# Optimization experiments

Hardware: AMD Instinct MI355X
Metric: run time of the kernel (lower is better)

Reference implementation:

```python
import jax, jax.numpy as jnp
import numpy as np

N = 50000        # num nodes
E = 800000       # num edges (avg degree 16)
IN = 64          # in_channels
H = 128          # hidden_channels
C1 = 64          # Num_TCN (fine clusters)
C2 = 16          # Num_TCN2 (coarse clusters)
DROP = 0.5       # drop_rate
THRESH = 1.0 / (C1 - 1)  # default edge_pruning_threshold
LN_EPS = 1e-5


def layer_norm(x, g, b):
    mu = jnp.mean(x, axis=-1, keepdims=True)
    var = jnp.var(x, axis=-1, keepdims=True)
    return (x - mu) * jax.lax.rsqrt(var + LN_EPS) * g + b


def graph_conv(x_src, row, col, W_rel, b, W_root, num_nodes):
    # PyG GraphConv (aggr='add'): out = lin_rel(sum_{src->dst} x[src]) + lin_root(x)
    agg = jax.ops.segment_sum(x_src[row], col, num_segments=num_nodes)
    return agg @ W_rel.T + b + x_src @ W_root.T


def mincut_common(x, s, A_s, deg):
    # shared tail of sparse_mincut_pool given A_s = A @ s and degree vector
    C = s.shape[-1]
    pooled_x = s.T @ x                                   # [C, F]
    pooled_adj = s.T @ A_s                               # [C, C]
    mincut_num = jnp.trace(pooled_adj)
    mincut_den = jnp.trace(s.T @ (deg[:, None] * s)) + 1e-10
    mincut_loss = -mincut_num / mincut_den
    sTs = s.T @ s
    norm = jnp.linalg.norm(sTs)
    ortho_loss = jnp.linalg.norm(sTs / (norm + 1e-10) - jnp.eye(C, dtype=x.dtype) / jnp.sqrt(jnp.asarray(C, x.dtype)))
    adj = pooled_adj * (1.0 - jnp.eye(C, dtype=x.dtype))  # fill_diagonal_(0)
    d_sqrt_inv = 1.0 / (jnp.sqrt(adj.sum(axis=1)) + 1e-15)
    adj_norm = adj * d_sqrt_inv[:, None] * d_sqrt_inv[None, :]
    return pooled_x, adj_norm, mincut_loss, ortho_loss


def mincut_sparse(x, row, col, s_logits, num_nodes):
    s = jax.nn.softmax(s_logits, axis=-1)
    # A_s[row] += s[col]  (edge_weight = 1) -> [N, C] scatter-add
    A_s = jax.ops.segment_sum(s[col], row, num_segments=num_nodes)
    deg = jax.ops.segment_sum(jnp.ones((row.shape[0],), x.dtype), row, num_segments=num_nodes)
    return mincut_common(x, s, A_s, deg)


def mincut_dense(x, M, s_logits):
    # pooled graph: dense 0/1 adjacency M[i,j]; equivalent to edge list from nonzero(M)
    s = jax.nn.softmax(s_logits, axis=-1)
    A_s = M @ s
    deg = M.sum(axis=1)
    return mincut_common(x, s, A_s, deg)


def setup_inputs() -> dict:
    key = jax.random.key(0)
    ks = jax.random.split(key, 12)
    x = jax.random.normal(ks[0], (N, IN), jnp.float32)
    edge_index = jax.random.randint(ks[1], (2, E), 0, N, jnp.int32)
    # bernoulli(1 - drop_rate) node-drop mask, fixed for determinism
    drop_mask = (jax.random.uniform(ks[2], (N,)) > DROP).astype(jnp.float32)
    p = lambda k, shp: (jax.random.normal(k, shp, jnp.float32) * 0.05)
    return dict(
        x=x, edge_index=edge_index, drop_mask=drop_mask,
        W1_rel=p(ks[3], (H, IN)), b1=jnp.zeros((H,), jnp.float32), W1_root=p(ks[4], (H, IN)),
        pW1=p(ks[5], (C1, H)), pb1=jnp.zeros((C1,), jnp.float32),
        g1=jnp.ones((C1,), jnp.float32), be1=jnp.zeros((C1,), jnp.float32),
        W2_rel=p(ks[6], (H, H)), b2=jnp.zeros((H,), jnp.float32), W2_root=p(ks[7], (H, H)),
        pW2=p(ks[8], (C2, H)), pb2=jnp.zeros((C2,), jnp.float32),
        g2=jnp.ones((C2,), jnp.float32), be2=jnp.zeros((C2,), jnp.float32),
    )


def reference(x, edge_index, drop_mask, W1_rel, b1, W1_root, pW1, pb1, g1, be1,
              W2_rel, b2, W2_root, pW2, pb2, g2, be2):
    # training=True path, S=1 (loss sums / S are identity)
    row, col = edge_index[0], edge_index[1]
    x_drop = drop_mask[:, None] * x
    x1 = jax.nn.relu(graph_conv(x_drop, row, col, W1_rel, b1, W1_root, N))   # [N, H]
    s1 = layer_norm(x1 @ pW1.T + pb1, g1, be1)                               # [N, C1]
    ls1 = jax.nn.log_softmax(s1, axis=-1)
    x_pool1, adj_pool1, mc1, o1 = mincut_sparse(x1, row, col, s1, N)
    # edge pruning -> dense 0/1 pooled adjacency (replaces nonzero + edge list)
    M = jnp.where(adj_pool1 > THRESH, 1.0, 0.0).astype(x.dtype)              # [C1, C1]
    # GraphConv on pooled graph: aggregate x[src] at dst == M.T @ x_pool1
    x2 = jax.nn.relu((M.T @ x_pool1) @ W2_rel.T + b2 + x_pool1 @ W2_root.T)  # [C1, H]
    s2 = layer_norm(x2 @ pW2.T + pb2, g2, be2)                               # [C1, C2]
    ls2 = jax.nn.log_softmax(s2, axis=-1)
    _, _, mc2, o2 = mincut_dense(x2, M, s2)
    return (mc1, o1, mc2, o2, ls1, ls2)
```

## Files before the change

### kernel.cpp

```cpp
#include <hip/hip_runtime.h>
#include <hip/hip_bf16.h>
#include <hip/hip_fp16.h>

#define NN 50000
#define NE 800000
#define INC 64
#define HC 128
#define NC1 64
#define NC2 16
#define DCAP 64

#define OFF_FLAG 0
#define OFW_W1R 16
#define OFW_W1O 8208
#define OFW_B1  16400
#define OFW_PW1 16528
#define OFW_PB1 24720
#define OFW_G1  24784
#define OFW_BE1 24848
#define OFW_W2R 24912
#define OFW_B2  41296
#define OFW_W2O 41424
#define OFW_PW2 57808
#define OFW_PB2 59856
#define OFW_G2  59872
#define OFW_BE2 59888
#define CVT_TOTAL 59888

#define OFW_PW1T 59904
#define OFF_MG   68096
#define OFF_MTG  72192
#define OFF_DEG2 76288
#define OFF_S2G  76352
#define OFW_WCT  77376
#define OFF_XD   127792
#define OFF_X1   3327792
#define OFF_S    9727792
#define OFF_AGG  12927792
#define OFF_CSRC 16127792
#define OFF_SCAL 17727792
#define OFF_PX   17727808
#define OFF_PADJ 17736000
#define OFF_STS  17740096
#define OFF_CUR  17744192
#define OFF_Q    17794192
#define OFF_END  17844192
#define ZERO_FLOATS (OFF_END - OFF_SCAL)

#define OFF_LOG    OFF_XD
#define OFF_PXSTSP OFF_XD
#define OFF_PADJP  OFF_X1
#define OFF_XD16   OFF_X1
#define OFF_S16    OFF_AGG
#define P_POOL 256
#define P_PADJ 1536
#define XSS 132

#define FC_G 2048
#define FC_SLICES (FC_G >> 3)
#define FC_ES ((NE + FC_SLICES - 1) / FC_SLICES)
#define FC_RANGE (NN >> 3)

__device__ inline float bflo(unsigned int u){ return __uint_as_float(u << 16); }
__device__ inline float bfhi(unsigned int u){ return __uint_as_float(u & 0xffff0000u); }

__device__ inline void store_out(void* out, long long idx, float v, bool bf){
  if (bf) ((__hip_bfloat16*)out)[idx] = __float2bfloat16(v);
  else    ((float*)out)[idx] = v;
}

__device__ inline float block_reduce_256(float v, float* red, int t){
  red[t] = v; __syncthreads();
#pragma unroll
  for (int sh = 128; sh > 0; sh >>= 1){
    if (t < sh) red[t] += red[t + sh];
    __syncthreads();
  }
  float r = red[0];
  __syncthreads();
  return r;
}

__global__ void k_detect(const unsigned int* __restrict__ dmw, float* __restrict__ flag){
  __shared__ int cnt;
  if (threadIdx.x == 0) cnt = 0;
  __syncthreads();
  int c = 0;
  for (int i = threadIdx.x; i < 12288; i += 256){
    unsigned int w = dmw[i];
    if (w == 0x3F803F80u || w == 0x00003F80u) c++;
  }
  atomicAdd(&cnt, c);
  __syncthreads();
  if (threadIdx.x == 0) flag[0] = (cnt > 64) ? 1.0f : 0.0f;
}

__global__ void k_cvt(const void* p0, const void* p1, const void* p2, const void* p3,
                      const void* p4, const void* p5, const void* p6, const void* p7,
                      const void* p8, const void* p9, const void* p10, const void* p11,
                      const void* p12, const void* p13,
                      const float* __restrict__ flag, float* __restrict__ ws){
  int i = blockIdx.x * blockDim.x + threadIdx.x;
  if (i >= CVT_TOTAL) return;
  const void* src; int off;
  if      (i < 8192 ){ src = p0;  off = i; }
  else if (i < 16384){ src = p1;  off = i - 8192; }
  else if (i < 16512){ src = p2;  off = i - 16384; }
  else if (i < 24704){ src = p3;  off = i - 16512; }
  else if (i < 24768){ src = p4;  off = i - 24704; }
  else if (i < 24832){ src = p5;  off = i - 24768; }
  else if (i < 24896){ src = p6;  off = i - 24832; }
  else if (i < 41280){ src = p7;  off = i - 24896; }
  else if (i < 41408){ src = p8;  off = i - 41280; }
  else if (i < 57792){ src = p9;  off = i - 41408; }
  else if (i < 59840){ src = p10; off = i - 57792; }
  else if (i < 59856){ src = p11; off = i - 59840; }
  else if (i < 59872){ src = p12; off = i - 59856; }
  else               { src = p13; off = i - 59872; }
  float v = (flag[0] > 0.5f) ? __bfloat162float(((const __hip_bfloat16*)src)[off])
                             : ((const float*)src)[off];
  ws[16 + i] = v;
  if (i < 8192){
    int h = i >> 6, j = i & 63;
    ws[OFW_WCT + j * 128 + h] = v;
  } else if (i < 16384){
    int o2 = i - 8192;
    int h = o2 >> 6, j = o2 & 63;
    ws[OFW_WCT + (64 + j) * 128 + h] = v;
  } else if (i >= 16512 && i < 24704){
    int o2 = i - 16512;
    int c = o2 >> 7, k = o2 & 127;
    ws[OFW_PW1T + k * 64 + c] = v;
  }
}

__global__ void k_xdrop(const void* __restrict__ xr, const void* __restrict__ dmr,
                        const float* __restrict__ flag, float* __restrict__ xd,
                        __half* __restrict__ xd16){
  int i4 = blockIdx.x * blockDim.x + threadIdx.x;
  if (i4 >= NN * 16) return;
  int n = i4 >> 4;
  float4 o;
  if (flag[0] > 0.5f){
    uint2 w = ((const uint2*)xr)[i4];
    float dv = __bfloat162float(((const __hip_bfloat16*)dmr)[n]);
    o.x = bflo(w.x) * dv; o.y = bfhi(w.x) * dv;
    o.z = bflo(w.y) * dv; o.w = bfhi(w.y) * dv;
  } else {
    float4 xv = ((const float4*)xr)[i4];
    float dv = ((const float*)dmr)[n];
    o.x = xv.x * dv; o.y = xv.y * dv; o.z = xv.z * dv; o.w = xv.w * dv;
  }
  ((float4*)xd)[i4] = o;
  __half2 ha = __floats2half2_rn(o.x, o.y);
  __half2 hb = __floats2half2_rn(o.z, o.w);
  uint2 hh;
  hh.x = *(unsigned int*)&ha;
  hh.y = *(unsigned int*)&hb;
  ((uint2*)xd16)[i4] = hh;
}

__global__ __launch_bounds__(256) void k_fillC(const int* __restrict__ ei, int* __restrict__ cur,
                        unsigned short* __restrict__ csrc2){
  int p = blockIdx.x & 7;
  int q = blockIdx.x >> 3;
  int lo = p * FC_RANGE;
  int base = q * FC_ES;
  int end = base + FC_ES; if (end > NE) end = NE;
  for (int e = base + (int)threadIdx.x; e < end; e += 256){
    int c = ei[NE + e];
    if ((unsigned)(c - lo) < (unsigned)FC_RANGE){
      int r = ei[e];
      int pos = atomicAdd(&cur[c], 1);
      if (pos < DCAP) csrc2[(c << 6) + pos] = (unsigned short)r;
    }
  }
}

#define G4ACC(Sq, Cq, Aq) \
    if (slot < Cq){ \
      uint2 u = *(const uint2*)(table + (Sq << 6) + (sub << 2)); \
      float2 f0 = __half22float2(*(__half2*)&u.x); \
      float2 f1 = __half22float2(*(__half2*)&u.y); \
      Aq.x += f0.x; Aq.y += f0.y; Aq.z += f1.x; Aq.w += f1.y; \
    }

__device__ inline void gather4h(const unsigned short* __restrict__ idx,
                                const int* __restrict__ cur,
                                int n0, const __half* __restrict__ table,
                                int lane, int g, int sub,
                                float4& A0, float4& A1, float4& A2, float4& A3){
  int c0 = cur[n0 + 0]; if (c0 > DCAP) c0 = DCAP;
  int c1 = cur[n0 + 1]; if (c1 > DCAP) c1 = DCAP;
  int c2 = cur[n0 + 2]; if (c2 > DCAP) c2 = DCAP;
  int c3 = cur[n0 + 3]; if (c3 > DCAP) c3 = DCAP;
  int my0 = (int)idx[((n0 + 0) << 6) + lane];
  int my1 = (int)idx[((n0 + 1) << 6) + lane];
  int my2 = (int)idx[((n0 + 2) << 6) + lane];
  int my3 = (int)idx[((n0 + 3) << 6) + lane];
  A0 = make_float4(0.f, 0.f, 0.f, 0.f); A1 = A0; A2 = A0; A3 = A0;
  int cmax = c0; if (c1 > cmax) cmax = c1; if (c2 > cmax) cmax = c2; if (c3 > cmax) cmax = c3;
#pragma unroll
  for (int i = 0; i < 4; ++i){
    int slot = g + (i << 2);
    int s0 = __shfl(my0, slot, 64);
    int s1 = __shfl(my1, slot, 64);
    int s2 = __shfl(my2, slot, 64);
    int s3 = __shfl(my3, slot, 64);
    G4ACC(s0, c0, A0)
    G4ACC(s1, c1, A1)
    G4ACC(s2, c2, A2)
    G4ACC(s3, c3, A3)
  }
  for (int i = 4; (i << 2) < cmax; ++i){
    int slot = g + (i << 2);
    int s0 = __shfl(my0, slot, 64);
    int s1 = __shfl(my1, slot, 64);
    int s2 = __shfl(my2, slot, 64);
    int s3 = __shfl(my3, slot, 64);
    G4ACC(s0, c0, A0)
    G4ACC(s1, c1, A1)
    G4ACC(s2, c2, A2)
    G4ACC(s3, c3, A3)
  }
}

__device__ inline void red4x(float4& A0, float4& A1, float4& A2, float4& A3){
#pragma unroll
  for (int o = 16; o < 64; o <<= 1){
    A0.x += __shfl_xor(A0.x, o, 64); A0.y += __shfl_xor(A0.y, o, 64);
    A0.z += __shfl_xor(A0.z, o, 64); A0.w += __shfl_xor(A0.w, o, 64);
    A1.x += __shfl_xor(A1.x, o, 64); A1.y += __shfl_xor(A1.y, o, 64);
    A1.z += __shfl_xor(A1.z, o, 64); A1.w += __shfl_xor(A1.w, o, 64);
    A2.x += __shfl_xor(A2.x, o, 64); A2.y += __shfl_xor(A2.y, o, 64);
    A2.z += __shfl_xor(A2.z, o, 64); A2.w += __shfl_xor(A2.w, o, 64);
    A3.x += __shfl_xor(A3.x, o, 64); A3.y += __shfl_xor(A3.y, o, 64);
    A3.z += __shfl_xor(A3.z, o, 64); A3.w += __shfl_xor(A3.w, o, 64);
  }
}

__global__ __launch_bounds__(256) void k_agg2(const int* __restrict__ cur,
                                              const unsigned short* __restrict__ csrc2,
                                              const __half* __restrict__ xd16,
                                              float* __restrict__ agg){
  int gid = blockIdx.x * 256 + threadIdx.x;
  int lane = gid & 63, wid = gid >> 6;
  int nw = (gridDim.x * 256) >> 6;
  int g = lane >> 4, sub = lane & 15;
  for (int nb = wid; nb < (NN >> 2); nb += nw){
    int n0 = nb << 2;
    float4 A0, A1, A2, A3;
    gather4h(csrc2, cur, n0, xd16, lane, g, sub, A0, A1, A2, A3);
    red4x(A0, A1, A2, A3);
    float4 W = (g == 0) ? A0 : (g == 1) ? A1 : (g == 2) ? A2 : A3;
    *(float4*)(agg + ((n0 + g) << 6) + (sub << 2)) = W;
  }
}

#define FMA4(ACC, AV) \
  ACC.x += AV.x*w0.x + AV.y*w1.x + AV.z*w2.x + AV.w*w3.x; \
  ACC.y += AV.x*w0.y + AV.y*w1.y + AV.z*w2.y + AV.w*w3.y; \
  ACC.z += AV.x*w0.z + AV.y*w1.z + AV.z*w2.z + AV.w*w3.z; \
  ACC.w += AV.x*w0.w + AV.y*w1.w + AV.z*w2.w + AV.w*w3.w;

__global__ __launch_bounds__(512, 2) void k_x1(const float* __restrict__ agg,
                                               const float* __restrict__ xd,
                                               const float* __restrict__ wts,
                                               float* __restrict__ x1){
  __shared__ __align__(16) float wt[128 * 128];
  __shared__ __align__(16) float at[64 * 128];
  int t = threadIdx.x;
  for (int f4 = t; f4 < 4096; f4 += 512)
    *(float4*)&wt[f4 << 2] = *(const float4*)&wts[OFW_WCT + (f4 << 2)];
  int ni = t >> 5;
  int cj = t & 31;
  float4 b4 = *(const float4*)&wts[OFW_B1 + (cj << 2)];
  const int ntiles = (NN + 63) >> 6;
  for (int tile = blockIdx.x; tile < ntiles; tile += gridDim.x){
    int base = tile << 6;
    __syncthreads();
    for (int f4 = t; f4 < 2048; f4 += 512){
      int i = f4 >> 5, kq = f4 & 31;
      int n = base + i;
      float4 v = make_float4(0.f, 0.f, 0.f, 0.f);
      if (n < NN){
        int k = kq << 2;
        v = (k < 64) ? *(const float4*)(agg + (n << 6) + k)
                     : *(const float4*)(xd  + (n << 6) + (k - 64));
      }
      *(float4*)&at[(i << 7) + (kq << 2)] = v;
    }
    __syncthreads();
    float4 acc0 = {0,0,0,0}, acc1 = {0,0,0,0}, acc2 = {0,0,0,0}, acc3 = {0,0,0,0};
    const float* ap = at + (ni << 9);
    const float* wp = wt + (cj << 2);
#pragma unroll 4
    for (int k = 0; k < 128; k += 4){
      float4 w0 = *(const float4*)(wp + ((k + 0) << 7));
      float4 w1 = *(const float4*)(wp + ((k + 1) << 7));
      float4 w2 = *(const float4*)(wp + ((k + 2) << 7));
      float4 w3 = *(const float4*)(wp + ((k + 3) << 7));
      float4 a0v = *(const float4*)(ap + k);
      float4 a1v = *(const float4*)(ap + 128 + k);
      float4 a2v = *(const float4*)(ap + 256 + k);
      float4 a3v = *(const float4*)(ap + 384 + k);
      FMA4(acc0, a0v)
      FMA4(acc1, a1v)
      FMA4(acc2, a2v)
      FMA4(acc3, a3v)
    }
    int n0 = base + (ni << 2);
    if (n0 + 0 < NN){
      float4 o; o.x = fmaxf(acc0.x + b4.x, 0.f); o.y = fmaxf(acc0.y + b4.y, 0.f);
      o.z = fmaxf(acc0.z + b4.z, 0.f); o.w = fmaxf(acc0.w + b4.w, 0.f);
      *(float4*)(x1 + (long long)(n0 + 0) * HC + (cj << 2)) = o;
    }
    if (n0 + 1 < NN){
      float4 o; o.x = fmaxf(acc1.x + b4.x, 0.f); o.y = fmaxf(acc1.y + b4.y, 0.f);
      o.z = fmaxf(acc1.z + b4.z, 0.f); o.w = fmaxf(acc1.w + b4.w, 0.f);
      *(float4*)(x1 + (long long)(n0 + 1) * HC + (cj << 2)) = o;
    }
    if (n0 + 2 < NN){
      float4 o; o.x = fmaxf(acc2.x + b4.x, 0.f); o.y = fmaxf(acc2.y + b4.y, 0.f);
      o.z = fmaxf(acc2.z + b4.z, 0.f); o.w = fmaxf(acc2.w + b4.w, 0.f);
      *(float4*)(x1 + (long long)(n0 + 2) * HC + (cj << 2)) = o;
    }
    if (n0 + 3 < NN){
      float4 o; o.x = fmaxf(acc3.x + b4.x, 0.f); o.y = fmaxf(acc3.y + b4.y, 0.f);
      o.z = fmaxf(acc3.z + b4.z, 0.f); o.w = fmaxf(acc3.w + b4.w, 0.f);
      *(float4*)(x1 + (long long)(n0 + 3) * HC + (cj << 2)) = o;
    }
  }
}

__global__ __launch_bounds__(512, 2) void k_s1g(const float* __restrict__ x1,
                                                const float* __restrict__ wts,
                                                float* __restrict__ logit){
  __shared__ __align__(16) float pw[128 * 64];
  __shared__ __align__(16) float at[64 * 128];
  int t = threadIdx.x;
  for (int f4 = t; f4 < 2048; f4 += 512)
    *(float4*)&pw[f4 << 2] = *(const float4*)&wts[OFW_PW1T + (f4 << 2)];
  int ni = t >> 5;
  int cj = t & 31;
  float2 pb = *(const float2*)&wts[OFW_PB1 + (cj << 1)];
  const int ntiles = (NN + 63) >> 6;
  for (int tile = blockIdx.x; tile < ntiles; tile += gridDim.x){
    int base = tile << 6;
    __syncthreads();
    for (int f4 = t; f4 < 2048; f4 += 512){
      int i = f4 >> 5, kq = f4 & 31;
      int n = base + i;
      float4 v = (n < NN) ? *(const float4*)(x1 + (long long)n * HC + (kq << 2))
                          : make_float4(0.f, 0.f, 0.f, 0.f);
      *(float4*)&at[(i << 7) + (kq << 2)] = v;
    }
    __syncthreads();
    float2 a0 = {0,0}, a1 = {0,0}, a2 = {0,0}, a3 = {0,0};
    const float* ap = at + (ni << 9);
    const float* wp = pw + (cj << 1);
#pragma unroll 4
    for (int k = 0; k < 128; k += 4){
      float2 w0 = *(const float2*)(wp + ((k + 0) << 6));
      float2 w1 = *(const float2*)(wp + ((k + 1) << 6));
      float2 w2 = *(const float2*)(wp + ((k + 2) << 6));
      float2 w3 = *(const float2*)(wp + ((k + 3) << 6));
      float4 x0 = *(const float4*)(ap + k);
      float4 x1v = *(const float4*)(ap + 128 + k);
      float4 x2v = *(const float4*)(ap + 256 + k);
      float4 x3v = *(const float4*)(ap + 384 + k);
      a0.x += x0.x*w0.x + x0.y*w1.x + x0.z*w2.x + x0.w*w3.x;
      a0.y += x0.x*w0.y + x0.y*w1.y + x0.z*w2.y + x0.w*w3.y;
      a1.x += x1v.x*w0.x + x1v.y*w1.x + x1v.z*w2.x + x1v.w*w3.x;
      a1.y += x1v.x*w0.y + x1v.y*w1.y + x1v.z*w2.y + x1v.w*w3.y;
      a2.x += x2v.x*w0.x + x2v.y*w1.x + x2v.z*w2.x + x2v.w*w3.x;
      a2.y += x2v.x*w0.y + x2v.y*w1.y + x2v.z*w2.y + x2v.w*w3.y;
      a3.x += x3v.x*w0.x + x3v.y*w1.x + x3v.z*w2.x + x3v.w*w3.x;
      a3.y += x3v.x*w0.y + x3v.y*w1.y + x3v.z*w2.y + x3v.w*w3.y;
    }
    int n0 = base + (ni << 2);
    if (n0 + 0 < NN){ float2 o; o.x = a0.x + pb.x; o.y = a0.y + pb.y;
      *(float2*)(logit + (long long)(n0 + 0) * 64 + (cj << 1)) = o; }
    if (n0 + 1 < NN){ float2 o; o.x = a1.x + pb.x; o.y = a1.y + pb.y;
      *(float2*)(logit + (long long)(n0 + 1) * 64 + (cj << 1)) = o; }
    if (n0 + 2 < NN){ float2 o; o.x = a2.x + pb.x; o.y = a2.y + pb.y;
      *(float2*)(logit + (long long)(n0 + 2) * 64 + (cj << 1)) = o; }
    if (n0 + 3 < NN){ float2 o; o.x = a3.x + pb.x; o.y = a3.y + pb.y;
      *(float2*)(logit + (long long)(n0 + 3) * 64 + (cj << 1)) = o; }
  }
}

__global__ __launch_bounds__(256) void k_lnsm(const float* __restrict__ logit,
                                              const float* __restrict__ wts,
                                              __half* __restrict__ s16,
                                              float* __restrict__ q,
                                              void* __restrict__ outp,
                                              const float* __restrict__ flag){
  int t = threadIdx.x;
  int lane = t & 63, wv = t >> 6;
  bool bf = flag[0] > 0.5f;
  float gl = wts[OFW_G1 + lane], bl = wts[OFW_BE1 + lane];
  int wg = blockIdx.x * 4 + wv;
  int nw = gridDim.x * 4;
  for (int r = wg * 4; r < NN; r += nw * 4){
    float z0 = logit[(long long)(r + 0) * 64 + lane];
    float z1 = logit[(long long)(r + 1) * 64 + lane];
    float z2 = logit[(long long)(r + 2) * 64 + lane];
    float z3 = logit[(long long)(r + 3) * 64 + lane];
    float s0 = z0, s1 = z1, s2 = z2, s3 = z3;
    float q0 = z0*z0, q1 = z1*z1, q2 = z2*z2, q3 = z3*z3;
#pragma unroll
    for (int o = 32; o > 0; o >>= 1){
      s0 += __shfl_xor(s0, o, 64); q0 += __shfl_xor(q0, o, 64);
      s1 += __shfl_xor(s1, o, 64); q1 += __shfl_xor(q1, o, 64);
      s2 += __shfl_xor(s2, o, 64); q2 += __shfl_xor(q2, o, 64);
      s3 += __shfl_xor(s3, o, 64); q3 += __shfl_xor(q3, o, 64);
    }
    float mu0 = s0 * 0.015625f, mu1 = s1 * 0.015625f;
    float mu2 = s2 * 0.015625f, mu3 = s3 * 0.015625f;
    float va0 = q0 * 0.015625f - mu0 * mu0;
    float va1 = q1 * 0.015625f - mu1 * mu1;
    float va2 = q2 * 0.015625f - mu2 * mu2;
    float va3 = q3 * 0.015625f - mu3 * mu3;
    float y0 = (z0 - mu0) * rsqrtf(va0 + 1e-5f) * gl + bl;
    float y1 = (z1 - mu1) * rsqrtf(va1 + 1e-5f) * gl + bl;
    float y2 = (z2 - mu2) * rsqrtf(va2 + 1e-5f) * gl + bl;
    float y3 = (z3 - mu3) * rsqrtf(va3 + 1e-5f) * gl + bl;
    float m0 = y0, m1 = y1, m2 = y2, m3 = y3;
#pragma unroll
    for (int o = 32; o > 0; o >>= 1){
      m0 = fmaxf(m0, __shfl_xor(m0, o, 64));
      m1 = fmaxf(m1, __shfl_xor(m1, o, 64));
      m2 = fmaxf(m2, __shfl_xor(m2, o, 64));
      m3 = fmaxf(m3, __shfl_xor(m3, o, 64));
    }
    float e0 = expf(y0 - m0), e1 = expf(y1 - m1);
    float e2 = expf(y2 - m2), e3 = expf(y3 - m3);
    float u0 = e0, u1 = e1, u2 = e2, u3 = e3;
    float w0 = e0*e0, w1 = e1*e1, w2 = e2*e2, w3 = e3*e3;
#pragma unroll
    for (int o = 32; o > 0; o >>= 1){
      u0 += __shfl_xor(u0, o, 64); w0 += __shfl_xor(w0, o, 64);
      u1 += __shfl_xor(u1, o, 64); w1 += __shfl_xor(w1, o, 64);
      u2 += __shfl_xor(u2, o, 64); w2 += __shfl_xor(w2, o, 64);
      u3 += __shfl_xor(u3, o, 64); w3 += __shfl_xor(w3, o, 64);
    }
    s16[(long long)(r + 0) * 64 + lane] = __float2half(e0 / u0);
    s16[(long long)(r + 1) * 64 + lane] = __float2half(e1 / u1);
    s16[(long long)(r + 2) * 64 + lane] = __float2half(e2 / u2);
    s16[(long long)(r + 3) * 64 + lane] = __float2half(e3 / u3);
    store_out(outp, 4LL + (long long)(r + 0) * 64 + lane, (y0 - m0) - logf(u0), bf);
    store_out(outp, 4LL + (long long)(r + 1) * 64 + lane, (y1 - m1) - logf(u1), bf);
    store_out(outp, 4LL + (long long)(r + 2) * 64 + lane, (y2 - m2) - logf(u2), bf);
    store_out(outp, 4LL + (long long)(r + 3) * 64 + lane, (y3 - m3) - logf(u3), bf);
    if (lane == 0){
      q[r + 0] = w0 / (u0 * u0);
      q[r + 1] = w1 / (u1 * u1);
      q[r + 2] = w2 / (u2 * u2);
      q[r + 3] = w3 / (u3 * u3);
    }
  }
}

__global__ __launch_bounds__(256) void k_den(const int* __restrict__ ei,
                                             const float* __restrict__ q,
                                             float* __restrict__ scal){
  __shared__ float red[256];
  int t = threadIdx.x;
  float acc = 0.0f;
  for (int e = blockIdx.x * 256 + t; e < NE; e += gridDim.x * 256)
    acc += q[ei[e]];
  float r = block_reduce_256(acc, red, t);
  if (t == 0) atomicAdd(&scal[0], r);
}

__global__ __launch_bounds__(256) void k_padj2(const int* __restrict__ cur,
                                               const unsigned short* __restrict__ csrc2,
                                               const __half* __restrict__ s16,
                                               float* __restrict__ padjp){
  __shared__ float rs[16 * 64];
  __shared__ float ra[16 * 64];
  int t = threadIdx.x, lane = t & 63, w = t >> 6;
  int g = lane >> 4, sub = lane & 15;
  int i4 = t >> 4;
  int j4 = t & 15;
  float4 acc0 = {0,0,0,0}, acc1 = {0,0,0,0}, acc2 = {0,0,0,0}, acc3 = {0,0,0,0};
  const int nbatch = NN / 16;
  for (int b = blockIdx.x; b < nbatch; b += gridDim.x){
    int base = b * 16;
    int n0 = base + (w << 2);
    float4 A0, A1, A2, A3;
    gather4h(csrc2, cur, n0, s16, lane, g, sub, A0, A1, A2, A3);
    uint2 ru = *(const uint2*)(s16 + ((n0 + g) << 6) + (sub << 2));
    float2 rf0 = __half22float2(*(__half2*)&ru.x), rf1 = __half22float2(*(__half2*)&ru.y);
    float4 R = make_float4(rf0.x, rf0.y, rf1.x, rf1.y);
    red4x(A0, A1, A2, A3);
    float4 W = (g == 0) ? A0 : (g == 1) ? A1 : (g == 2) ? A2 : A3;
    int k = (w << 2) + g;
    *(float4*)&rs[k * 64 + (sub << 2)] = W;
    *(float4*)&ra[k * 64 + (sub << 2)] = R;
    __syncthreads();
#pragma unroll
    for (int kk = 0; kk < 16; ++kk){
      float4 a  = *(const float4*)&rs[kk * 64 + (i4 << 2)];
      float4 bv = *(const float4*)&ra[kk * 64 + (j4 << 2)];
      acc0.x += a.x * bv.x; acc0.y += a.x * bv.y; acc0.z += a.x * bv.z; acc0.w += a.x * bv.w;
      acc1.x += a.y * bv.x; acc1.y += a.y * bv.y; acc1.z += a.y * bv.z; acc1.w += a.y * bv.w;
      acc2.x += a.z * bv.x; acc2.y += a.z * bv.y; acc2.z += a.z * bv.z; acc2.w += a.z * bv.w;
      acc3.x += a.w * bv.x; acc3.y += a.w * bv.y; acc3.z += a.w * bv.z; acc3.w += a.w * bv.w;
    }
    __syncthreads();
  }
  float* pp = padjp + blockIdx.x * 4096;
  *(float4*)&pp[(i4 * 4 + 0) * 64 + (j4 << 2)] = acc0;
  *(float4*)&pp[(i4 * 4 + 1) * 64 + (j4 << 2)] = acc1;
  *(float4*)&pp[(i4 * 4 + 2) * 64 + (j4 << 2)] = acc2;
  *(float4*)&pp[(i4 * 4 + 3) * 64 + (j4 << 2)] = acc3;
}

__global__ __launch_bounds__(1024) void k_pool(const __half* __restrict__ s16,
                                               const float* __restrict__ x1,
                                               float* __restrict__ part){
  __shared__ float ssh[32 * 64];
  __shared__ float xsh[32 * 128];
  int t = threadIdx.x;
  int c = t >> 4, q = t & 15;
  float4 apx0 = {0,0,0,0}, apx1 = {0,0,0,0}, ast0 = {0,0,0,0};
  const int nbatch = (NN + 31) / 32;
  for (int b = blockIdx.x; b < nbatch; b += gridDim.x){
    int base = b * 32;
    int kmax = NN - base; if (kmax > 32) kmax = 32;
    if (t < 512){
      int k = t >> 4, col = t & 15;
      float4 v = make_float4(0.f, 0.f, 0.f, 0.f);
      if (k < kmax){
        uint2 u = *(const uint2*)(s16 + ((base + k) << 6) + (col << 2));
        float2 f0 = __half22float2(*(__half2*)&u.x), f1 = __half22float2(*(__half2*)&u.y);
        v = make_float4(f0.x, f0.y, f1.x, f1.y);
      }
      *(float4*)&ssh[k * 64 + (col << 2)] = v;
    }
    {
      int k = t >> 5, col = t & 31;
      float4 v = (k < kmax) ? *(const float4*)(x1 + (base + k) * HC + (col << 2))
                            : make_float4(0, 0, 0, 0);
      *(float4*)&xsh[k * 128 + (col << 2)] = v;
    }
    __syncthreads();
    for (int k = 0; k < kmax; ++k){
      float sv = ssh[k * 64 + c];
      float4 xv0 = *(const float4*)&xsh[k * 128 + (q << 2)];
      float4 xv1 = *(const float4*)&xsh[k * 128 + ((q + 16) << 2)];
      float4 s0  = *(const float4*)&ssh[k * 64 + (q << 2)];
      apx0.x += sv * xv0.x; apx0.y += sv * xv0.y; apx0.z += sv * xv0.z; apx0.w += sv * xv0.w;
      apx1.x += sv * xv1.x; apx1.y += sv * xv1.y; apx1.z += sv * xv1.z; apx1.w += sv * xv1.w;
      ast0.x += sv * s0.x;  ast0.y += sv * s0.y;  ast0.z += sv * s0.z;  ast0.w += sv * s0.w;
    }
    __syncthreads();
  }
  float* pp = part + blockIdx.x * 12288;
  *(float4*)&pp[c * 128 + (q << 2)]        = apx0;
  *(float4*)&pp[c * 128 + ((q + 16) << 2)] = apx1;
  *(float4*)&pp[8192 + c * 64 + (q << 2)]  = ast0;
}

__global__ __launch_bounds__(256) void k_red(const float* __restrict__ pxstsp,
                                             const float* __restrict__ padjp,
                                             float* __restrict__ px,
                                             float* __restrict__ sts,
                                             float* __restrict__ padj){
  __shared__ float sh[256];
  int b = blockIdx.x, t = threadIdx.x;
  int ci = t & 63, pc = t >> 6;
  if (b < 192){
    int cell = b * 64 + ci;
    float a0 = 0, a1 = 0, a2 = 0, a3 = 0;
    const float* basep = pxstsp + cell;
    int p0 = pc * (P_POOL / 4);
    for (int p = 0; p < P_POOL / 4; p += 4){
      a0 += basep[(p0 + p    ) * 12288];
      a1 += basep[(p0 + p + 1) * 12288];
      a2 += basep[(p0 + p + 2) * 12288];
      a3 += basep[(p0 + p + 3) * 12288];
    }
    sh[t] = (a0 + a1) + (a2 + a3);
    __syncthreads();
    if (t < 64){
      float r = sh[t] + sh[t + 64] + sh[t + 128] + sh[t + 192];
      int cell2 = b * 64 + t;
      if (cell2 < 8192) px[cell2] = r; else sts[cell2 - 8192] = r;
    }
  } else {
    int cell = (b - 192) * 64 + ci;
    float a0 = 0, a1 = 0, a2 = 0, a3 = 0;
    const float* basep = padjp + cell;
    int p0 = pc * (P_PADJ / 4);
    for (int p = 0; p < P_PADJ / 4; p += 4){
      a0 += basep[(p0 + p    ) * 4096];
      a1 += basep[(p0 + p + 1) * 4096];
      a2 += basep[(p0 + p + 2) * 4096];
      a3 += basep[(p0 + p + 3) * 4096];
    }
    sh[t] = (a0 + a1) + (a2 + a3);
    __syncthreads();
    if (t < 64) padj[(b - 192) * 64 + t] = sh[t] + sh[t + 64] + sh[t + 128] + sh[t + 192];
  }
}

__global__ __launch_bounds__(256) void k_m(const float* __restrict__ padj,
                                           const float* __restrict__ sts,
                                           float* __restrict__ Mg,
                                           float* __restrict__ Mtg,
                                           float* __restrict__ deg2,
                                           float* __restrict__ scal){
  __shared__ float red[256];
  __shared__ float psh[4096];
  __shared__ float dsi[64];
  int t = threadIdx.x;
  const float TH = 1.0f / 63.0f;
  for (int i = t; i < 4096; i += 256) psh[i] = padj[i];
  __syncthreads();
  float v = (t < 64) ? psh[t * 65] : 0.0f;
  float num1 = block_reduce_256(v, red, t);
  v = 0.0f;
  for (int i = t; i < 4096; i += 256){ float e = sts[i]; v += e * e; }
  float nrm1 = sqrtf(block_reduce_256(v, red, t));
  v = 0.0f;
  for (int i = t; i < 4096; i += 256){
    float e = sts[i] / (nrm1 + 1e-10f) - ((i % 65 == 0) ? 0.125f : 0.0f);
    v += e * e;
  }
  float o1 = sqrtf(block_reduce_256(v, red, t));
  if (t < 64){
    float rs = 0.0f;
    for (int j = 0; j < 64; ++j) rs += (j == t) ? 0.0f : psh[t * 64 + j];
    dsi[t] = 1.0f / (sqrtf(rs) + 1e-15f);
  }
  __syncthreads();
  for (int i = t; i < 4096; i += 256){
    int r = i >> 6, c = i & 63;
    float a = (r == c) ? 0.0f : psh[i];
    float m = (a * dsi[r] * dsi[c] > TH) ? 1.0f : 0.0f;
    Mg[i] = m;
    Mtg[c * 64 + r] = m;
  }
  __syncthreads();
  for (int i = t; i < 4096; i += 256){
    int r = i >> 6, c = i & 63;
    float a = (r == c) ? 0.0f : psh[i];
    psh[i] = (a * dsi[r] * dsi[c] > TH) ? 1.0f : 0.0f;
  }
  __syncthreads();
  if (t < 64){
    float d2 = 0.0f;
    for (int j = 0; j < 64; ++j) d2 += psh[t * 64 + j];
    deg2[t] = d2;
  }
  if (t == 0){ scal[1] = num1; scal[2] = o1; }
}

__global__ __launch_bounds__(128) void k_x2(const float* __restrict__ Mtg,
                                            const float* __restrict__ px,
                                            const float* __restrict__ wts,
                                            float* __restrict__ s2g,
                                            void* __restrict__ out,
                                            const float* __restrict__ flag){
  __shared__ float mt[64], pxc[128], mpsh[128], x2sh[128];
  __shared__ float part[16][9], lsh[16], stat[2];
  int c = blockIdx.x, t = threadIdx.x;
  if (t < 64) mt[t] = Mtg[c * 64 + t];
  pxc[t] = px[c * 128 + t];
  __syncthreads();
  float mp = 0.0f;
  for (int i = 0; i < 64; ++i) mp += mt[i] * px[i * 128 + t];
  mpsh[t] = mp;
  __syncthreads();
  float acc = wts[OFW_B2 + t];
  const float* wrr = wts + OFW_W2R + t * 128;
  const float* wor = wts + OFW_W2O + t * 128;
  for (int k = 0; k < 128; ++k) acc += mpsh[k] * wrr[k] + pxc[k] * wor[k];
  x2sh[t] = fmaxf(acc, 0.0f);
  __syncthreads();
  { int u = t >> 3, p = t & 7;
    const float* pw = wts + OFW_PW2 + u * 128 + p * 16;
    float pa = 0.0f;
    for (int k = 0; k < 16; ++k) pa += x2sh[p * 16 + k] * pw[k];
    part[u][p] = pa;
  }
  __syncthreads();
  if (t < 16){
    float l = wts[OFW_PB2 + t];
    for (int p = 0; p < 8; ++p) l += part[t][p];
    lsh[t] = l;
  }
  __syncthreads();
  if (t == 0){
    float mu = 0.0f;
    for (int u = 0; u < 16; ++u) mu += lsh[u];
    mu *= (1.0f / 16.0f);
    float var = 0.0f;
    for (int u = 0; u < 16; ++u){ float d = lsh[u] - mu; var += d * d; }
    var *= (1.0f / 16.0f);
    float rstd = rsqrtf(var + 1e-5f);
    float m = -3.4e38f;
    for (int u = 0; u < 16; ++u){
      lsh[u] = (lsh[u] - mu) * rstd * wts[OFW_G2 + u] + wts[OFW_BE2 + u];
      m = fmaxf(m, lsh[u]);
    }
    float se = 0.0f;
    for (int u = 0; u < 16; ++u) se += expf(lsh[u] - m);
    stat[0] = m; stat[1] = logf(se);
  }
  __syncthreads();
  if (t < 16){
    float ls = (lsh[t] - stat[0]) - stat[1];
    store_out(out, 4LL + (long long)NN * NC1 + c * 16 + t, ls, flag[0] > 0.5f);
    s2g[c * 16 + t] = expf(ls);
  }
}

__global__ __launch_bounds__(256) void k_tail(const float* __restrict__ Mg,
                                              const float* __restrict__ s2g,
                                              const float* __restrict__ deg2,
                                              const float* __restrict__ scal,
                                              void* __restrict__ out,
                                              const float* __restrict__ flag){
  __shared__ float red[256];
  __shared__ float Msh[4096];
  __shared__ float s2sh[1024];
  __shared__ float d2sh[64];
  __shared__ float sts2[256];
  int t = threadIdx.x;
  for (int i = t; i < 4096; i += 256) Msh[i] = Mg[i];
  for (int i = t; i < 1024; i += 256) s2sh[i] = s2g[i];
  if (t < 64) d2sh[t] = deg2[t];
  __syncthreads();
  float vnum = 0.0f, vden = 0.0f;
  for (int m = 0; m < 4; ++m){
    int id = t + m * 256;
    int c = id >> 4, u = id & 15;
    float a = 0.0f;
    for (int j = 0; j < 64; ++j) a += Msh[c * 64 + j] * s2sh[j * 16 + u];
    float sv = s2sh[id];
    vnum += sv * a;
    vden += d2sh[c] * sv * sv;
  }
  float num2 = block_reduce_256(vnum, red, t);
  float den2 = block_reduce_256(vden, red, t) + 1e-10f;
  { int u = t >> 4, w = t & 15;
    float a = 0.0f;
    for (int c2 = 0; c2 < 64; ++c2) a += s2sh[c2 * 16 + u] * s2sh[c2 * 16 + w];
    sts2[t] = a;
  }
  __syncthreads();
  float v = sts2[t] * sts2[t];
  float nrm2 = sqrtf(block_reduce_256(v, red, t));
  { float e = sts2[t] / (nrm2 + 1e-10f) - (((t >> 4) == (t & 15)) ? 0.25f : 0.0f);
    v = e * e; }
  float o2 = sqrtf(block_reduce_256(v, red, t));
  if (t == 0){
    bool bf = flag[0] > 0.5f;
    float den = scal[0] + 1e-10f;
    store_out(out, 0, -scal[1] / den, bf);
    store_out(out, 1, scal[2], bf);
    store_out(out, 2, -num2 / den2, bf);
    store_out(out, 3, o2, bf);
  }
}

extern "C" void kernel_launch(void* const* d_in, const int* in_sizes, int n_in,
                              void* d_out, int out_size, void* d_ws, size_t ws_size,
                              hipStream_t stream){
  const void* x  = d_in[0];
  const int*  ei = (const int*)d_in[1];
  const void* dm = d_in[2];

  float* ws    = (float*)d_ws;
  float* flag  = ws + OFF_FLAG;
  float* xd    = ws + OFF_XD;
  float* x1    = ws + OFF_X1;
  float* agg   = ws + OFF_AGG;
  float* px    = ws + OFF_PX;
  float* padj  = ws + OFF_PADJ;
  float* sts   = ws + OFF_STS;
  float* scal  = ws + OFF_SCAL;
  float* Mg    = ws + OFF_MG;
  float* Mtg   = ws + OFF_MTG;
  float* deg2  = ws + OFF_DEG2;
  float* s2g   = ws + OFF_S2G;
  float* q     = ws + OFF_Q;
  float* logit = ws + OFF_LOG;
  float* pxstsp= ws + OFF_PXSTSP;
  float* padjp = ws + OFF_PADJP;
  __half* xd16 = (__half*)(ws + OFF_XD16);
  __half* s16  = (__half*)(ws + OFF_S16);
  unsigned short* csrc2 = (unsigned short*)(ws + OFF_CSRC);
  int* cur = (int*)(ws + OFF_CUR);

  hipMemsetAsync(ws + OFF_SCAL, 0, (size_t)ZERO_FLOATS * sizeof(float), stream);

  k_detect<<<1, 256, 0, stream>>>((const unsigned int*)dm, flag);
  k_cvt<<<(CVT_TOTAL + 255) / 256, 256, 0, stream>>>(
      d_in[3], d_in[5], d_in[4], d_in[6], d_in[7], d_in[8], d_in[9],
      d_in[10], d_in[11], d_in[12], d_in[13], d_in[14], d_in[15], d_in[16],
      flag, ws);
  k_xdrop<<<(NN * 16 + 255) / 256, 256, 0, stream>>>(x, dm, flag, xd, xd16);
  k_fillC<<<FC_G, 256, 0, stream>>>(ei, cur, csrc2);
  k_agg2<<<2048, 256, 0, stream>>>(cur, csrc2, xd16, agg);
  k_x1<<<256, 512, 0, stream>>>(agg, xd, ws, x1);
  k_s1g<<<512, 512, 0, stream>>>(x1, ws, logit);
  k_lnsm<<<1024, 256, 0, stream>>>(logit, ws, s16, q, d_out, flag);
  k_den<<<256, 256, 0, stream>>>(ei, q, scal);
  k_pool<<<P_POOL, 1024, 0, stream>>>(s16, x1, pxstsp);
  k_padj2<<<P_PADJ, 256, 0, stream>>>(cur, csrc2, s16, padjp);
  k_red<<<256, 256, 0, stream>>>(pxstsp, padjp, px, sts, padj);
  k_m<<<1, 256, 0, stream>>>(padj, sts, Mg, Mtg, deg2, scal);
  k_x2<<<64, 128, 0, stream>>>(Mtg, px, ws, s2g, d_out, flag);
  k_tail<<<1, 256, 0, stream>>>(Mg, s2g, deg2, scal, d_out, flag);
}
```

Baseline: 388.5 us.

## Pack aggregate and dropped features into one fp16 buffer; use fdot2 in first GraphConv

The dropped input x and its neighbour aggregate are now stored side by side as fp16 in one 128-wide row per node, replacing separate fp32 buffers. k_x1 stages these fp16 rows and fp16 packed weights in LDS and computes the first GraphConv with v_dot2 fp16 instructions. With less LDS it raises launch bounds to 4 blocks per CU and launches one block per tile. This halves the traffic for writing and reading agg and xd and shrinks shared memory, but it rounds the aggregate and weights to fp16, which loses some accuracy.

Result: faster. 374.8 us (median of 2 runs) (-3.5%).

```diff
diff --git a/kernel.cpp b/kernel.cpp
--- a/kernel.cpp
+++ b/kernel.cpp
@@ -32,10 +32,9 @@
 #define OFF_MTG  72192
 #define OFF_DEG2 76288
 #define OFF_S2G  76352
-#define OFW_WCT  77376
+#define OFW_WCT16 93760
 #define OFF_XD   127792
 #define OFF_X1   3327792
-#define OFF_S    9727792
 #define OFF_AGG  12927792
 #define OFF_CSRC 16127792
 #define OFF_SCAL 17727792
@@ -50,11 +49,10 @@
 #define OFF_LOG    OFF_XD
 #define OFF_PXSTSP OFF_XD
 #define OFF_PADJP  OFF_X1
-#define OFF_XD16   OFF_X1
+#define OFF_AX16   OFF_AGG
 #define OFF_S16    OFF_AGG
 #define P_POOL 256
 #define P_PADJ 1536
-#define XSS 132
 
 #define FC_G 2048
 #define FC_SLICES (FC_G >> 3)
@@ -63,6 +61,11 @@
 
 __device__ inline float bflo(unsigned int u){ return __uint_as_float(u << 16); }
 __device__ inline float bfhi(unsigned int u){ return __uint_as_float(u & 0xffff0000u); }
+
+typedef _Float16 h2t __attribute__((ext_vector_type(2)));
+__device__ inline float dot2f(unsigned int a, unsigned int w, float c){
+  return __builtin_amdgcn_fdot2(__builtin_bit_cast(h2t, a), __builtin_bit_cast(h2t, w), c, false);
+}
 
 __device__ inline void store_out(void* out, long long idx, float v, bool bf){
   if (bf) ((__hip_bfloat16*)out)[idx] = __float2bfloat16(v);
@@ -120,13 +123,14 @@
   float v = (flag[0] > 0.5f) ? __bfloat162float(((const __hip_bfloat16*)src)[off])
                              : ((const float*)src)[off];
   ws[16 + i] = v;
+  __half* w16 = (__half*)(ws + OFW_WCT16);
   if (i < 8192){
     int h = i >> 6, j = i & 63;
-    ws[OFW_WCT + j * 128 + h] = v;
+    w16[(j >> 1) * 256 + h * 2 + (j & 1)] = __float2half(v);
   } else if (i < 16384){
     int o2 = i - 8192;
     int h = o2 >> 6, j = o2 & 63;
-    ws[OFW_WCT + (64 + j) * 128 + h] = v;
+    w16[(32 + (j >> 1)) * 256 + h * 2 + (j & 1)] = __float2half(v);
   } else if (i >= 16512 && i < 24704){
     int o2 = i - 16512;
     int c = o2 >> 7, k = o2 & 127;
@@ -135,11 +139,11 @@
 }
 
 __global__ void k_xdrop(const void* __restrict__ xr, const void* __restrict__ dmr,
-                        const float* __restrict__ flag, float* __restrict__ xd,
-                        __half* __restrict__ xd16){
+                        const float* __restrict__ flag, __half* __restrict__ ax16){
   int i4 = blockIdx.x * blockDim.x + threadIdx.x;
   if (i4 >= NN * 16) return;
   int n = i4 >> 4;
+  int c0 = (i4 & 15) << 2;
   float4 o;
   if (flag[0] > 0.5f){
     uint2 w = ((const uint2*)xr)[i4];
@@ -151,13 +155,12 @@
     float dv = ((const float*)dmr)[n];
     o.x = xv.x * dv; o.y = xv.y * dv; o.z = xv.z * dv; o.w = xv.w * dv;
   }
-  ((float4*)xd)[i4] = o;
   __half2 ha = __floats2half2_rn(o.x, o.y);
   __half2 hb = __floats2half2_rn(o.z, o.w);
   uint2 hh;
   hh.x = *(unsigned int*)&ha;
   hh.y = *(unsigned int*)&hb;
-  ((uint2*)xd16)[i4] = hh;
+  *(uint2*)(ax16 + ((long long)n << 7) + 64 + c0) = hh;
 }
 
 __global__ __launch_bounds__(256) void k_fillC(const int* __restrict__ ei, int* __restrict__ cur,
@@ -179,12 +182,13 @@
 
 #define G4ACC(Sq, Cq, Aq) \
     if (slot < Cq){ \
-      uint2 u = *(const uint2*)(table + (Sq << 6) + (sub << 2)); \
+      uint2 u = *(const uint2*)(table + ((Sq) << RSH) + COFF + (sub << 2)); \
       float2 f0 = __half22float2(*(__half2*)&u.x); \
       float2 f1 = __half22float2(*(__half2*)&u.y); \
       Aq.x += f0.x; Aq.y += f0.y; Aq.z += f1.x; Aq.w += f1.y; \
     }
 
+template<int RSH, int COFF>
 __device__ inline void gather4h(const unsigned short* __restrict__ idx,
                                 const int* __restrict__ cur,
                                 int n0, const __half* __restrict__ table,
@@ -241,8 +245,7 @@
 
 __global__ __launch_bounds__(256) void k_agg2(const int* __restrict__ cur,
                                               const unsigned short* __restrict__ csrc2,
-                                              const __half* __restrict__ xd16,
-                                              float* __restrict__ agg){
+                                              __half* __restrict__ ax16){
   int gid = blockIdx.x * 256 + threadIdx.x;
   int lane = gid & 63, wid = gid >> 6;
   int nw = (gridDim.x * 256) >> 6;
@@ -250,28 +253,39 @@
   for (int nb = wid; nb < (NN >> 2); nb += nw){
     int n0 = nb << 2;
     float4 A0, A1, A2, A3;
-    gather4h(csrc2, cur, n0, xd16, lane, g, sub, A0, A1, A2, A3);
+    gather4h<7, 64>(csrc2, cur, n0, ax16, lane, g, sub, A0, A1, A2, A3);
     red4x(A0, A1, A2, A3);
     float4 W = (g == 0) ? A0 : (g == 1) ? A1 : (g == 2) ? A2 : A3;
-    *(float4*)(agg + ((n0 + g) << 6) + (sub << 2)) = W;
-  }
-}
-
-#define FMA4(ACC, AV) \
-  ACC.x += AV.x*w0.x + AV.y*w1.x + AV.z*w2.x + AV.w*w3.x; \
-  ACC.y += AV.x*w0.y + AV.y*w1.y + AV.z*w2.y + AV.w*w3.y; \
-  ACC.z += AV.x*w0.z + AV.y*w1.z + AV.z*w2.z + AV.w*w3.z; \
-  ACC.w += AV.x*w0.w + AV.y*w1.w + AV.z*w2.w + AV.w*w3.w;
-
-__global__ __launch_bounds__(512, 2) void k_x1(const float* __restrict__ agg,
-                                               const float* __restrict__ xd,
+    __half2 h0 = __floats2half2_rn(W.x, W.y);
+    __half2 h1 = __floats2half2_rn(W.z, W.w);
+    uint2 hh;
+    hh.x = *(unsigned int*)&h0;
+    hh.y = *(unsigned int*)&h1;
+    *(uint2*)(ax16 + ((long long)(n0 + g) << 7) + (sub << 2)) = hh;
+  }
+}
+
+#define DOT16(ACC, AV) \
+  ACC.x = dot2f(AV.x, w0.x, ACC.x); ACC.x = dot2f(AV.y, w1.x, ACC.x); \
+  ACC.x = dot2f(AV.z, w2.x, ACC.x); ACC.x = dot2f(AV.w, w3.x, ACC.x); \
+  ACC.y = dot2f(AV.x, w0.y, ACC.y); ACC.y = dot2f(AV.y, w1.y, ACC.y); \
+  ACC.y = dot2f(AV.z, w2.y, ACC.y); ACC.y = dot2f(AV.w, w3.y, ACC.y); \
+  ACC.z = dot2f(AV.x, w0.z, ACC.z); ACC.z = dot2f(AV.y, w1.z, ACC.z); \
+  ACC.z = dot2f(AV.z, w2.z, ACC.z); ACC.z = dot2f(AV.w, w3.z, ACC.z); \
+  ACC.w = dot2f(AV.x, w0.w, ACC.w); ACC.w = dot2f(AV.y, w1.w, ACC.w); \
+  ACC.w = dot2f(AV.z, w2.w, ACC.w); ACC.w = dot2f(AV.w, w3.w, ACC.w);
+
+__global__ __launch_bounds__(512, 4) void k_x1(const __half* __restrict__ ax16,
                                                const float* __restrict__ wts,
                                                float* __restrict__ x1){
-  __shared__ __align__(16) float wt[128 * 128];
-  __shared__ __align__(16) float at[64 * 128];
+  __shared__ __align__(16) unsigned int wt16[64 * 128];
+  __shared__ __align__(16) __half at16[64 * 128];
   int t = threadIdx.x;
-  for (int f4 = t; f4 < 4096; f4 += 512)
-    *(float4*)&wt[f4 << 2] = *(const float4*)&wts[OFW_WCT + (f4 << 2)];
+  {
+    const uint4* wsrc = (const uint4*)((const unsigned int*)(wts + OFW_WCT16));
+    for (int f4 = t; f4 < 2048; f4 += 512)
+      *(uint4*)&wt16[f4 << 2] = wsrc[f4];
+  }
   int ni = t >> 5;
   int cj = t & 31;
   float4 b4 = *(const float4*)&wts[OFW_B1 + (cj << 2)];
@@ -279,35 +293,31 @@
   for (int tile = blockIdx.x; tile < ntiles; tile += gridDim.x){
     int base = tile << 6;
     __syncthreads();
-    for (int f4 = t; f4 < 2048; f4 += 512){
-      int i = f4 >> 5, kq = f4 & 31;
-      int n = base + i;
-      float4 v = make_float4(0.f, 0.f, 0.f, 0.f);
-      if (n < NN){
-        int k = kq << 2;
-        v = (k < 64) ? *(const float4*)(agg + (n << 6) + k)
-                     : *(const float4*)(xd  + (n << 6) + (k - 64));
-      }
-      *(float4*)&at[(i << 7) + (kq << 2)] = v;
+    {
+      const uint4* src = (const uint4*)(ax16 + ((long long)base << 7));
+      uint4 v0 = src[t << 1];
+      uint4 v1 = src[(t << 1) | 1];
+      *(uint4*)&at16[t << 4] = v0;
+      *(uint4*)&at16[(t << 4) | 8] = v1;
     }
     __syncthreads();
     float4 acc0 = {0,0,0,0}, acc1 = {0,0,0,0}, acc2 = {0,0,0,0}, acc3 = {0,0,0,0};
-    const float* ap = at + (ni << 9);
-    const float* wp = wt + (cj << 2);
+    const __half* ap = at16 + (ni << 9);
+    const unsigned int* wp = wt16 + (cj << 2);
 #pragma unroll 4
-    for (int k = 0; k < 128; k += 4){
-      float4 w0 = *(const float4*)(wp + ((k + 0) << 7));
-      float4 w1 = *(const float4*)(wp + ((k + 1) << 7));
-      float4 w2 = *(const float4*)(wp + ((k + 2) << 7));
-      float4 w3 = *(const float4*)(wp + ((k + 3) << 7));
-      float4 a0v = *(const float4*)(ap + k);
-      float4 a1v = *(const float4*)(ap + 128 + k);
-      float4 a2v = *(const float4*)(ap + 256 + k);
-      float4 a3v = *(const float4*)(ap + 384 + k);
-      FMA4(acc0, a0v)
-      FMA4(acc1, a1v)
-      FMA4(acc2, a2v)
-      FMA4(acc3, a3v)
+    for (int kb = 0; kb < 16; ++kb){
+      uint4 w0 = *(const uint4*)(wp + (((kb << 2) + 0) << 7));
+      uint4 w1 = *(const uint4*)(wp + (((kb << 2) + 1) << 7));
+      uint4 w2 = *(const uint4*)(wp + (((kb << 2) + 2) << 7));
+      uint4 w3 = *(const uint4*)(wp + (((kb << 2) + 3) << 7));
+      uint4 a0 = *(const uint4*)(ap + (kb << 3));
+      uint4 a1 = *(const uint4*)(ap + 128 + (kb << 3));
+      uint4 a2 = *(const uint4*)(ap + 256 + (kb << 3));
+      uint4 a3 = *(const uint4*)(ap + 384 + (kb << 3));
+      DOT16(acc0, a0)
+      DOT16(acc1, a1)
+      DOT16(acc2, a2)
+      DOT16(acc3, a3)
     }
     int n0 = base + (ni << 2);
     if (n0 + 0 < NN){
@@ -490,7 +500,7 @@
     int base = b * 16;
     int n0 = base + (w << 2);
     float4 A0, A1, A2, A3;
-    gather4h(csrc2, cur, n0, s16, lane, g, sub, A0, A1, A2, A3);
+    gather4h<6, 0>(csrc2, cur, n0, s16, lane, g, sub, A0, A1, A2, A3);
     uint2 ru = *(const uint2*)(s16 + ((n0 + g) << 6) + (sub << 2));
     float2 rf0 = __half22float2(*(__half2*)&ru.x), rf1 = __half22float2(*(__half2*)&ru.y);
     float4 R = make_float4(rf0.x, rf0.y, rf1.x, rf1.y);
@@ -777,9 +787,7 @@
 
   float* ws    = (float*)d_ws;
   float* flag  = ws + OFF_FLAG;
-  float* xd    = ws + OFF_XD;
   float* x1    = ws + OFF_X1;
-  float* agg   = ws + OFF_AGG;
   float* px    = ws + OFF_PX;
   float* padj  = ws + OFF_PADJ;
   float* sts   = ws + OFF_STS;
@@ -792,7 +800,7 @@
   float* logit = ws + OFF_LOG;
   float* pxstsp= ws + OFF_PXSTSP;
   float* padjp = ws + OFF_PADJP;
-  __half* xd16 = (__half*)(ws + OFF_XD16);
+  __half* ax16 = (__half*)(ws + OFF_AX16);
   __half* s16  = (__half*)(ws + OFF_S16);
   unsigned short* csrc2 = (unsigned short*)(ws + OFF_CSRC);
   int* cur = (int*)(ws + OFF_CUR);
@@ -804,10 +812,10 @@
       d_in[3], d_in[5], d_in[4], d_in[6], d_in[7], d_in[8], d_in[9],
       d_in[10], d_in[11], d_in[12], d_in[13], d_in[14], d_in[15], d_in[16],
       flag, ws);
-  k_xdrop<<<(NN * 16 + 255) / 256, 256, 0, stream>>>(x, dm, flag, xd, xd16);
+  k_xdrop<<<(NN * 16 + 255) / 256, 256, 0, stream>>>(x, dm, flag, ax16);
   k_fillC<<<FC_G, 256, 0, stream>>>(ei, cur, csrc2);
-  k_agg2<<<2048, 256, 0, stream>>>(cur, csrc2, xd16, agg);
-  k_x1<<<256, 512, 0, stream>>>(agg, xd, ws, x1);
+  k_agg2<<<2048, 256, 0, stream>>>(cur, csrc2, ax16);
+  k_x1<<<782, 512, 0, stream>>>(ax16, ws, x1);
   k_s1g<<<512, 512, 0, stream>>>(x1, ws, logit);
   k_lnsm<<<1024, 256, 0, stream>>>(logit, ws, s16, q, d_out, flag);
   k_den<<<256, 256, 0, stream>>>(ei, q, scal);
```
